# Performance work log

Measured on AMD Instinct MI355X. Metric: run time of the kernel, lower is better.

Reference implementation:

```python
import jax, jax.numpy as jnp
import numpy as np

# ---- config (matches init_kwargs) ----
NUM_HEADS = 8
HEAD_DIM = 48
IN_CH = 384
OUT_CH = 384
AGENTS_HW = (7, 7)
CLUSTERS_HW = (2, 2)
NUM_MODULES = 2          # ['PartitionalClustering', 'FuzzyClustering']
N_GROUPS = 1 + 2 * NUM_MODULES   # p + (k, v) per module
D = NUM_HEADS * HEAD_DIM          # 384
NUM_CLUSTERS = CLUSTERS_HW[0] * CLUSTERS_HW[1]   # 4 per module
NUM_ALL_CLUSTERS = NUM_MODULES * NUM_CLUSTERS    # 8
EPS = 1e-6


def adaptive_avg_pool(x, oh, ow):
    # x: [b, c, H, W], H % oh == 0, W % ow == 0 -> exact block mean
    b, c, H, W = x.shape
    return x.reshape(b, c, oh, H // oh, ow, W // ow).mean(axis=(3, 5))


def setup_inputs() -> dict:
    key = jax.random.key(0)
    ks = jax.random.split(key, 6)
    B, H, W = 16, 56, 56
    x = jax.random.normal(ks[0], (B, IN_CH, H, W), dtype=jnp.float32)
    # proj: 1x1 linear in_channels -> N_GROUPS * D
    proj_w = jax.random.normal(ks[1], (N_GROUPS * D, IN_CH), dtype=jnp.float32) * (IN_CH ** -0.5)
    proj_b = jnp.zeros((N_GROUPS * D,), dtype=jnp.float32)
    sim_alpha = jnp.ones((NUM_ALL_CLUSTERS,), dtype=jnp.float32)
    sim_beta = jnp.zeros((NUM_ALL_CLUSTERS,), dtype=jnp.float32)
    proj2_w = jax.random.normal(ks[2], (OUT_CH, D), dtype=jnp.float32) * (D ** -0.5)
    proj2_b = jnp.zeros((OUT_CH,), dtype=jnp.float32)
    return {"x": x, "proj_w": proj_w, "proj_b": proj_b,
            "sim_alpha": sim_alpha, "sim_beta": sim_beta,
            "proj2_w": proj2_w, "proj2_b": proj2_b}


def _cluster_attention(i, k, v, kc, vc):
    # k: [b, c, Na] agent keys; v: [b, Na, c] agent values
    # kc, vc: [b, M, c] cluster centroids (keys / values)
    c = k.shape[1]
    scores = jnp.einsum('bmc,bcn->bmn', kc, k) / jnp.sqrt(jnp.float32(c))  # [b, M, Na]
    if i == 0:  # PartitionalClustering: attend over tokens per centroid
        attn = jax.nn.softmax(scores, axis=-1)
        agg = jnp.einsum('bmn,bnc->bmc', attn, v)
    else:       # FuzzyClustering: soft membership over clusters, normalized average
        memb = jax.nn.softmax(scores, axis=1)                              # over clusters
        agg = jnp.einsum('bmn,bnc->bmc', memb, v) / (memb.sum(axis=-1, keepdims=True) + EPS)
    return agg + vc  # with_cluster_bias=True


def reference(x, proj_w, proj_b, sim_alpha, sim_beta, proj2_w, proj2_b):
    B, C, H, W = x.shape
    # proj (1x1 linear over channels)
    y = jnp.einsum('bchw,oc->bohw', x, proj_w) + proj_b[None, :, None, None]
    y = y.reshape(B, N_GROUPS, D, H, W).transpose(1, 0, 2, 3, 4)
    b = B * NUM_HEADS
    c = HEAD_DIM
    y = y.reshape(N_GROUPS, b, c, H, W)
    p, r = y[0], y[1:]
    r = r.reshape(NUM_MODULES, 2, b, c, H, W)

    ah, aw = AGENTS_HW
    na = ah * aw
    agg_list = []
    for i in range(NUM_MODULES):  # fixed small structural loop
        k_full, v_full = r[i, 0], r[i, 1]
        kc = adaptive_avg_pool(k_full, *CLUSTERS_HW).reshape(b, c, NUM_CLUSTERS).transpose(0, 2, 1)
        vc = adaptive_avg_pool(v_full, *CLUSTERS_HW).reshape(b, c, NUM_CLUSTERS).transpose(0, 2, 1)
        k = adaptive_avg_pool(k_full, ah, aw).reshape(b, c, na)             # [b, c, Na]
        v = adaptive_avg_pool(v_full, ah, aw).reshape(b, c, na).transpose(0, 2, 1)  # [b, Na, c]
        agg_list.append(_cluster_attention(i, k, v, kc, vc))
    agg = jnp.concatenate(agg_list, axis=1)  # [b, M_all, c]

    p_agents = adaptive_avg_pool(p, ah, aw).reshape(b, c, na)  # [b, c, Na]
    # cosine similarity between centroid aggregates and query tokens
    agg_n = agg / (jnp.linalg.norm(agg, axis=-1, keepdims=True) + EPS)
    p_n = p_agents / (jnp.linalg.norm(p_agents, axis=1, keepdims=True) + EPS)
    sim = jnp.einsum('bmc,bcn->bmn', agg_n, p_n)  # [b, M_all, Na]
    similarity = sim_alpha[None, :, None] * sim + sim_beta[None, :, None]
    assignment = jax.nn.softmax(similarity, axis=1)  # over clusters

    out = jnp.einsum('bmc,bmn->bcn', agg, assignment)  # [b, c, Na]
    out = out.reshape(b, c, ah, aw)
    # bilinear upsample (half-pixel centers == torch align_corners=False)
    out = jax.image.resize(out, (b, c, H, W), method='linear')
    out = out.reshape(B, D, H, W)
    out = jnp.einsum('bdhw,od->bohw', out, proj2_w) + proj2_b[None, :, None, None]
    return out
```

## Files before the change

kernel.cpp:

```cpp
#include <hip/hip_runtime.h>
#include <math.h>

#define CIN    384
#define NPIX   3136

typedef float vf4 __attribute__((ext_vector_type(4)));
typedef __attribute__((ext_vector_type(4))) float f32x4;
typedef __attribute__((ext_vector_type(8))) short bf16x8;
typedef __attribute__((ext_vector_type(8))) unsigned short u16x8;

__device__ __forceinline__ unsigned short f2bf(float f) {
    unsigned u = __float_as_uint(f);
    u = (u + 0x7FFF + ((u >> 16) & 1)) >> 16;
    return (unsigned short)u;
}
__device__ __forceinline__ float bf2f(unsigned short h) {
    return __uint_as_float(((unsigned)h) << 16);
}

__global__ __launch_bounds__(256) void k_front(const float* __restrict__ x,
                                               const float* __restrict__ W,
                                               unsigned short* __restrict__ Xhi,
                                               unsigned short* __restrict__ Xlo,
                                               unsigned short* __restrict__ Whi,
                                               unsigned short* __restrict__ Wlo) {
    int blk = blockIdx.x;
    int t = threadIdx.x;
    if (blk >= 6144) {
        int i = (blk - 6144) * 256 + t;
        float w = W[i];
        unsigned short hi = f2bf(w);
        Whi[i] = hi;
        Wlo[i] = f2bf(w - bf2f(hi));
        return;
    }
    int Bi = blk / CIN;
    int ch = blk - Bi * CIN;
    __shared__ float ps[56][14];
    __shared__ float s14[14][14];
    const float* xp = x + (size_t)(Bi * CIN + ch) * NPIX;
    for (int p = t; p < 784; p += 256) {
        int row = p / 14, cb = p % 14;
        const vf4 v = __builtin_nontemporal_load(
            reinterpret_cast<const vf4*>(xp + row * 56 + cb * 4));
        ps[row][cb] = v.x + v.y + v.z + v.w;
    }
    __syncthreads();
    if (t < 196) {
        int ri = t / 14, cb = t % 14;
        s14[ri][cb] = ps[4*ri][cb] + ps[4*ri+1][cb] + ps[4*ri+2][cb] + ps[4*ri+3][cb];
    }
    __syncthreads();
    if (t < 49) {
        int i = t / 7, j = t % 7;
        float s = (s14[2*i][2*j] + s14[2*i][2*j+1] + s14[2*i+1][2*j] + s14[2*i+1][2*j+1])
                  * (1.0f / 64.0f);
        int p = Bi * 49 + t;
        unsigned short hi = f2bf(s);
        Xhi[(size_t)p * 384 + ch] = hi;
        Xlo[(size_t)p * 384 + ch] = f2bf(s - bf2f(hi));
    } else if (t >= 64 && t < 68) {
        int m = t - 64;
        int mi = m / 2, mj = m % 2;
        float s = 0.f;
        for (int ri = 7*mi; ri < 7*mi + 7; ++ri)
            for (int cb = 7*mj; cb < 7*mj + 7; ++cb)
                s += s14[ri][cb];
        s *= (1.0f / 784.0f);
        int p = 784 + Bi * 4 + m;
        unsigned short hi = f2bf(s);
        Xhi[(size_t)p * 384 + ch] = hi;
        Xlo[(size_t)p * 384 + ch] = f2bf(s - bf2f(hi));
    }
}

__global__ __launch_bounds__(512) void k_fuse(
        const unsigned short* __restrict__ Whi, const unsigned short* __restrict__ Wlo,
        const unsigned short* __restrict__ Xhi, const unsigned short* __restrict__ Xlo,
        const float* __restrict__ proj_b,
        const float* __restrict__ alpha, const float* __restrict__ beta,
        float* __restrict__ osT) {
    int bb = blockIdx.x;
    int Bi = bb >> 3, head = bb & 7;
    __shared__ float yT[16560];
    __shared__ float e0[4][49], memb[4][49];
    __shared__ float rowmax0[4], esum0[4], msum[4];
    __shared__ float agg[8][48];
    __shared__ float anorm[8], pnorm[49];
    __shared__ float simL[8][49];
    __shared__ float assignW[8][49];
    unsigned short* sAh = (unsigned short*)yT;
    unsigned short* sAl = sAh + 9600;
    unsigned short* sBh = sAl + 9600;
    unsigned short* sBl = sBh + 2560;
    int t = threadIdx.x;
    int lane = t & 63, w = t >> 6;
    int fr = lane & 15, fq = lane >> 4;

    int row0 = t >> 2, ko0 = (t & 3) * 8;
    int g0 = row0 / 48, cc0 = row0 - g0 * 48;
    size_t aoff0 = (size_t)(g0 * 384 + head * 48 + cc0) * 384 + ko0;
    int c1 = t + 512;
    int row1 = c1 >> 2, ko1 = (c1 & 3) * 8;
    int g1 = row1 / 48, cc1 = row1 - g1 * 48;
    size_t aoff1 = (size_t)(g1 * 384 + head * 48 + cc1) * 384 + ko1;
    int bko = (t & 3) * 8;
    int brow = t >> 2;
    int bp = brow < 49 ? Bi * 49 + brow : 784 + Bi * 4 + (brow - 49);
    size_t boff = (size_t)bp * 384 + bko;

    u16x8 rAh0, rAl0, rAh1, rAl1, rBh, rBl;
    rAh0 = *(const u16x8*)(Whi + aoff0);
    rAl0 = *(const u16x8*)(Wlo + aoff0);
    if (t < 448) { rAh1 = *(const u16x8*)(Whi + aoff1); rAl1 = *(const u16x8*)(Wlo + aoff1); }
    if (t < 212) { rBh  = *(const u16x8*)(Xhi + boff);  rBl  = *(const u16x8*)(Xlo + boff); }

    f32x4 acc[2][4] = {};
    for (int step = 0; step < 12; ++step) {
        *(u16x8*)&sAh[row0 * 40 + ko0] = rAh0;
        *(u16x8*)&sAl[row0 * 40 + ko0] = rAl0;
        if (t < 448) {
            *(u16x8*)&sAh[row1 * 40 + ko1] = rAh1;
            *(u16x8*)&sAl[row1 * 40 + ko1] = rAl1;
        }
        if (t < 212) {
            *(u16x8*)&sBh[brow * 40 + bko] = rBh;
            *(u16x8*)&sBl[brow * 40 + bko] = rBl;
        }
        __syncthreads();
        if (step < 11) {
            int k0 = (step + 1) * 32;
            rAh0 = *(const u16x8*)(Whi + aoff0 + k0);
            rAl0 = *(const u16x8*)(Wlo + aoff0 + k0);
            if (t < 448) { rAh1 = *(const u16x8*)(Whi + aoff1 + k0); rAl1 = *(const u16x8*)(Wlo + aoff1 + k0); }
            if (t < 212) { rBh  = *(const u16x8*)(Xhi + boff + k0);  rBl  = *(const u16x8*)(Xlo + boff + k0); }
        }
        bf16x8 bh[4], bl[4];
#pragma unroll
        for (int nt = 0; nt < 4; ++nt) {
            int r = nt * 16 + fr;
            bh[nt] = *(const bf16x8*)&sBh[r * 40 + fq * 8];
            bl[nt] = *(const bf16x8*)&sBl[r * 40 + fq * 8];
        }
#pragma unroll
        for (int mi = 0; mi < 2; ++mi) {
            int mt = 2 * w + mi;
            if (mt < 15) {
                int r = mt * 16 + fr;
                bf16x8 ah = *(const bf16x8*)&sAh[r * 40 + fq * 8];
                bf16x8 al = *(const bf16x8*)&sAl[r * 40 + fq * 8];
#pragma unroll
                for (int nt = 0; nt < 4; ++nt) {
                    acc[mi][nt] = __builtin_amdgcn_mfma_f32_16x16x32_bf16(ah, bh[nt], acc[mi][nt], 0, 0, 0);
                    acc[mi][nt] = __builtin_amdgcn_mfma_f32_16x16x32_bf16(ah, bl[nt], acc[mi][nt], 0, 0, 0);
                    acc[mi][nt] = __builtin_amdgcn_mfma_f32_16x16x32_bf16(al, bh[nt], acc[mi][nt], 0, 0, 0);
                }
            }
        }
        __syncthreads();
    }
#pragma unroll
    for (int mi = 0; mi < 2; ++mi) {
        int mt = 2 * w + mi;
        if (mt < 15) {
#pragma unroll
            for (int j = 0; j < 4; ++j) {
                int m = mt * 16 + fq * 4 + j;
                int g = m / 48, cc = m - g * 48;
                float bb = proj_b[g * 384 + head * 48 + cc];
#pragma unroll
                for (int nt = 0; nt < 4; ++nt)
                    yT[m * 69 + nt * 16 + fr] = acc[mi][nt][j] + bb;
            }
        }
    }
    __syncthreads();

    const float scale = 0.14433756729740643f;
    if (t < 392) {
        int i = t / 196, r = t % 196;
        int m = r / 49, n = r % 49;
        int rbase = 48 + 96 * i;
        float s = 0.f;
        for (int cc = 0; cc < 48; ++cc)
            s += yT[(rbase + cc) * 69 + 49 + m] * yT[(rbase + cc) * 69 + n];
        s *= scale;
        if (i == 0) e0[m][n] = s; else memb[m][n] = s;
    }
    __syncthreads();
    if (t < 4) {
        float mx = -1e30f;
        for (int n = 0; n < 49; ++n) mx = fmaxf(mx, e0[t][n]);
        rowmax0[t] = mx;
    }
    __syncthreads();
    if (t < 196) { int m = t / 49, n = t % 49; e0[m][n] = expf(e0[m][n] - rowmax0[m]); }
    __syncthreads();
    if (t < 4) { float s = 0.f; for (int n = 0; n < 49; ++n) s += e0[t][n]; esum0[t] = s; }
    if (t >= 64 && t < 113) {
        int n = t - 64;
        float a0 = memb[0][n], a1 = memb[1][n], a2 = memb[2][n], a3 = memb[3][n];
        float mx = fmaxf(fmaxf(a0, a1), fmaxf(a2, a3));
        float x0 = expf(a0 - mx), x1 = expf(a1 - mx), x2 = expf(a2 - mx), x3 = expf(a3 - mx);
        float s = x0 + x1 + x2 + x3;
        memb[0][n] = x0 / s; memb[1][n] = x1 / s; memb[2][n] = x2 / s; memb[3][n] = x3 / s;
    }
    __syncthreads();
    if (t < 4) { float s = 0.f; for (int n = 0; n < 49; ++n) s += memb[t][n]; msum[t] = s; }
    __syncthreads();
    if (t < 384) {
        int row = t / 48, cc = t % 48;
        float a = 0.f;
        if (row < 4) {
            const float* vr = &yT[(96 + cc) * 69];
            for (int n = 0; n < 49; ++n) a += e0[row][n] * vr[n];
            agg[row][cc] = a / esum0[row] + vr[49 + row];
        } else {
            int m = row - 4;
            const float* vr = &yT[(192 + cc) * 69];
            for (int n = 0; n < 49; ++n) a += memb[m][n] * vr[n];
            agg[row][cc] = a / (msum[m] + 1e-6f) + vr[49 + m];
        }
    }
    __syncthreads();
    if (t < 8) {
        float s = 0.f;
        for (int cc = 0; cc < 48; ++cc) { float a = agg[t][cc]; s += a * a; }
        anorm[t] = sqrtf(s) + 1e-6f;
    }
    if (t >= 64 && t < 113) {
        int n = t - 64; float s = 0.f;
        for (int cc = 0; cc < 48; ++cc) { float a = yT[cc * 69 + n]; s += a * a; }
        pnorm[n] = sqrtf(s) + 1e-6f;
    }
    __syncthreads();
    if (t < 392) {
        int m = t / 49, n = t - m * 49;
        float dot = 0.f;
        for (int cc = 0; cc < 48; ++cc) dot += agg[m][cc] * yT[cc * 69 + n];
        simL[m][n] = alpha[m] * (dot / (anorm[m] * pnorm[n])) + beta[m];
    }
    __syncthreads();
    if (t < 49) {
        int n = t;
        float mx = -1e30f, e[8];
        for (int m = 0; m < 8; ++m) mx = fmaxf(mx, simL[m][n]);
        float ssum = 0.f;
        for (int m = 0; m < 8; ++m) { e[m] = expf(simL[m][n] - mx); ssum += e[m]; }
        float inv = 1.f / ssum;
        for (int m = 0; m < 8; ++m) assignW[m][n] = e[m] * inv;
    }
    __syncthreads();
    for (int idx = t; idx < 2352; idx += 512) {
        int n = idx / 48, cc = idx - n * 48;
        float s = 0.f;
        for (int m = 0; m < 8; ++m) s += agg[m][cc] * assignW[m][n];
        osT[((size_t)(Bi * 49 + n)) * 384 + head * 48 + cc] = s;
    }
}

__global__ __launch_bounds__(256) void k_upf(const float* __restrict__ osT,
                                             const float* __restrict__ W2,
                                             const float* __restrict__ b2,
                                             float* __restrict__ out) {
    int blk = blockIdx.x;
    int Bi = blk / 96, cg = blk - Bi * 96;
    int ch0 = cg * 4;
    __shared__ float W2L[4 * 388];
    __shared__ float OsL[49 * 100];
    __shared__ float zL[4][52];
    __shared__ float tmp[4][56][8];
    int t = threadIdx.x;
    for (int i = t; i < 1536; i += 256)
        W2L[(i / 384) * 388 + (i % 384)] = W2[(size_t)ch0 * 384 + i];
    int c = t & 3, n = t >> 2;
    float acc = 0.f;
    for (int kc = 0; kc < 4; ++kc) {
        __syncthreads();
        for (int i = t; i < 49 * 24; i += 256) {
            int nn = i / 24, j = i - nn * 24;
            float4 f = *reinterpret_cast<const float4*>(
                osT + ((size_t)(Bi * 49 + nn)) * 384 + kc * 96 + j * 4);
            *reinterpret_cast<float4*>(&OsL[nn * 100 + j * 4]) = f;
        }
        __syncthreads();
        if (t < 196) {
            const float* wrow = W2L + c * 388 + kc * 96;
            const float* orow = OsL + n * 100;
#pragma unroll
            for (int j = 0; j < 24; ++j) {
                float4 wv = *reinterpret_cast<const float4*>(wrow + j * 4);
                float4 ov = *reinterpret_cast<const float4*>(orow + j * 4);
                acc += wv.x * ov.x + wv.y * ov.y + wv.z * ov.z + wv.w * ov.w;
            }
        }
    }
    __syncthreads();
    if (t < 196) zL[c][n] = acc + b2[ch0 + c];
    __syncthreads();
    for (int idx = t; idx < 1568; idx += 256) {
        int cc = idx / 392, rem = idx - cc * 392;
        int h = rem / 7, iw = rem - h * 7;
        float sh = (h - 3.5f) * 0.125f;
        int ih0; float fh;
        if (sh <= 0.f)      { ih0 = 0; fh = 0.f; }
        else if (sh >= 6.f) { ih0 = 6; fh = 0.f; }
        else                { ih0 = (int)sh; fh = sh - (float)ih0; }
        int ih1 = min(ih0 + 1, 6);
        float z0 = zL[cc][ih0 * 7 + iw];
        tmp[cc][h][iw] = z0 + fh * (zL[cc][ih1 * 7 + iw] - z0);
    }
    __syncthreads();
    size_t obase = ((size_t)(Bi * 384 + ch0)) * (size_t)NPIX;
    for (int q = t; q < 3136; q += 256) {
        int cc = q / 784, rem = q - cc * 784;
        int h = rem / 14, qw = rem - h * 14;
        const float* tr = &tmp[cc][h][0];
        vf4 o4;
#pragma unroll
        for (int j = 0; j < 4; ++j) {
            int w = qw * 4 + j;
            float sw = (w - 3.5f) * 0.125f;
            int iw0; float fw;
            if (sw <= 0.f)      { iw0 = 0; fw = 0.f; }
            else if (sw >= 6.f) { iw0 = 6; fw = 0.f; }
            else                { iw0 = (int)sw; fw = sw - (float)iw0; }
            int iw1 = min(iw0 + 1, 6);
            float t0 = tr[iw0];
            o4[j] = t0 + fw * (tr[iw1] - t0);
        }
        __builtin_nontemporal_store(o4,
            reinterpret_cast<vf4*>(out + obase + (size_t)q * 4));
    }
}

extern "C" void kernel_launch(void* const* d_in, const int* in_sizes, int n_in,
                              void* d_out, int out_size, void* d_ws, size_t ws_size,
                              hipStream_t stream) {
    const float* x      = (const float*)d_in[0];
    const float* proj_w = (const float*)d_in[1];
    const float* proj_b = (const float*)d_in[2];
    const float* alpha  = (const float*)d_in[3];
    const float* beta   = (const float*)d_in[4];
    const float* w2     = (const float*)d_in[5];
    const float* b2     = (const float*)d_in[6];
    float* out = (float*)d_out;
    float* ws  = (float*)d_ws;

    float* osT = ws;
    unsigned short* Whi = (unsigned short*)(ws + (size_t)301056);
    unsigned short* Wlo = (unsigned short*)(ws + (size_t)669696);
    unsigned short* Xhi = (unsigned short*)(ws + (size_t)1038336);
    unsigned short* Xlo = (unsigned short*)(ws + (size_t)1210368);

    k_front<<<dim3(9024), 256, 0, stream>>>(x, proj_w, Xhi, Xlo, Whi, Wlo);
    k_fuse <<<dim3(128),  512, 0, stream>>>(Whi, Wlo, Xhi, Xlo, proj_b, alpha, beta, osT);
    k_upf  <<<dim3(1536), 256, 0, stream>>>(osT, w2, b2, out);
}
```

Before: 81.17 us.

## Move proj2 GEMM onto split-bf16 MFMA kernel ahead of upsample

After: 74.36 us. 8.4% less time.

```diff
diff --git a/kernel.cpp b/kernel.cpp
--- a/kernel.cpp
+++ b/kernel.cpp
@@ -19,19 +19,30 @@
 }
 
 __global__ __launch_bounds__(256) void k_front(const float* __restrict__ x,
-                                               const float* __restrict__ W,
+                                               const float* __restrict__ W1,
+                                               const float* __restrict__ W2,
                                                unsigned short* __restrict__ Xhi,
                                                unsigned short* __restrict__ Xlo,
-                                               unsigned short* __restrict__ Whi,
-                                               unsigned short* __restrict__ Wlo) {
+                                               unsigned short* __restrict__ Whi1,
+                                               unsigned short* __restrict__ Wlo1,
+                                               unsigned short* __restrict__ Whi2,
+                                               unsigned short* __restrict__ Wlo2) {
     int blk = blockIdx.x;
     int t = threadIdx.x;
+    if (blk >= 9024) {
+        int i = (blk - 9024) * 256 + t;
+        float w = W2[i];
+        unsigned short hi = f2bf(w);
+        Whi2[i] = hi;
+        Wlo2[i] = f2bf(w - bf2f(hi));
+        return;
+    }
     if (blk >= 6144) {
         int i = (blk - 6144) * 256 + t;
-        float w = W[i];
+        float w = W1[i];
         unsigned short hi = f2bf(w);
-        Whi[i] = hi;
-        Wlo[i] = f2bf(w - bf2f(hi));
+        Whi1[i] = hi;
+        Wlo1[i] = f2bf(w - bf2f(hi));
         return;
     }
     int Bi = blk / CIN;
@@ -79,7 +90,7 @@
         const unsigned short* __restrict__ Xhi, const unsigned short* __restrict__ Xlo,
         const float* __restrict__ proj_b,
         const float* __restrict__ alpha, const float* __restrict__ beta,
-        float* __restrict__ osT) {
+        unsigned short* __restrict__ osThi, unsigned short* __restrict__ osTlo) {
     int bb = blockIdx.x;
     int Bi = bb >> 3, head = bb & 7;
     __shared__ float yT[16560];
@@ -251,55 +262,84 @@
         for (int m = 0; m < 8; ++m) assignW[m][n] = e[m] * inv;
     }
     __syncthreads();
-    for (int idx = t; idx < 2352; idx += 512) {
+    for (int idx = t; idx < 3072; idx += 512) {
         int n = idx / 48, cc = idx - n * 48;
         float s = 0.f;
-        for (int m = 0; m < 8; ++m) s += agg[m][cc] * assignW[m][n];
-        osT[((size_t)(Bi * 49 + n)) * 384 + head * 48 + cc] = s;
-    }
-}
-
-__global__ __launch_bounds__(256) void k_upf(const float* __restrict__ osT,
-                                             const float* __restrict__ W2,
+        if (n < 49)
+            for (int m = 0; m < 8; ++m) s += agg[m][cc] * assignW[m][n];
+        size_t o = ((size_t)(Bi * 64 + n)) * 384 + head * 48 + cc;
+        unsigned short hi = f2bf(s);
+        osThi[o] = hi;
+        osTlo[o] = f2bf(s - bf2f(hi));
+    }
+}
+
+__global__ __launch_bounds__(512) void k_gemm2m(
+        const unsigned short* __restrict__ Whi2, const unsigned short* __restrict__ Wlo2,
+        const unsigned short* __restrict__ osThi, const unsigned short* __restrict__ osTlo,
+        float* __restrict__ z) {
+    int blk = blockIdx.x;
+    int Bi = blk / 3, rg = blk - Bi * 3;
+    __shared__ unsigned short sAh[128 * 40], sAl[128 * 40];
+    __shared__ unsigned short sBh[64 * 40],  sBl[64 * 40];
+    int t = threadIdx.x;
+    int lane = t & 63, w = t >> 6;
+    int fr = lane & 15, fq = lane >> 4;
+    int arow = t >> 2, ako = (t & 3) * 8;
+    size_t aoff = (size_t)(rg * 128 + arow) * 384 + ako;
+    int brow = (t & 255) >> 2, bko = (t & 3) * 8;
+    size_t boff = ((size_t)(Bi * 64 + brow)) * 384 + bko;
+    f32x4 acc[4] = {};
+    for (int k0 = 0; k0 < 384; k0 += 32) {
+        *(u16x8*)&sAh[arow * 40 + ako] = *(const u16x8*)(Whi2 + aoff + k0);
+        *(u16x8*)&sAl[arow * 40 + ako] = *(const u16x8*)(Wlo2 + aoff + k0);
+        if (t < 256) {
+            *(u16x8*)&sBh[brow * 40 + bko] = *(const u16x8*)(osThi + boff + k0);
+            *(u16x8*)&sBl[brow * 40 + bko] = *(const u16x8*)(osTlo + boff + k0);
+        }
+        __syncthreads();
+        int r = w * 16 + fr;
+        bf16x8 ah = *(const bf16x8*)&sAh[r * 40 + fq * 8];
+        bf16x8 al = *(const bf16x8*)&sAl[r * 40 + fq * 8];
+#pragma unroll
+        for (int nt = 0; nt < 4; ++nt) {
+            int rb = nt * 16 + fr;
+            bf16x8 bh = *(const bf16x8*)&sBh[rb * 40 + fq * 8];
+            bf16x8 bl = *(const bf16x8*)&sBl[rb * 40 + fq * 8];
+            acc[nt] = __builtin_amdgcn_mfma_f32_16x16x32_bf16(ah, bh, acc[nt], 0, 0, 0);
+            acc[nt] = __builtin_amdgcn_mfma_f32_16x16x32_bf16(ah, bl, acc[nt], 0, 0, 0);
+            acc[nt] = __builtin_amdgcn_mfma_f32_16x16x32_bf16(al, bh, acc[nt], 0, 0, 0);
+        }
+        __syncthreads();
+    }
+#pragma unroll
+    for (int j = 0; j < 4; ++j) {
+        int ch = rg * 128 + w * 16 + fq * 4 + j;
+#pragma unroll
+        for (int nt = 0; nt < 4; ++nt) {
+            int col = nt * 16 + fr;
+            if (col < 49)
+                z[((size_t)(Bi * 384 + ch)) * 52 + col] = acc[nt][j];
+        }
+    }
+}
+
+__global__ __launch_bounds__(256) void k_up4(const float* __restrict__ z,
                                              const float* __restrict__ b2,
                                              float* __restrict__ out) {
     int blk = blockIdx.x;
     int Bi = blk / 96, cg = blk - Bi * 96;
     int ch0 = cg * 4;
-    __shared__ float W2L[4 * 388];
-    __shared__ float OsL[49 * 100];
     __shared__ float zL[4][52];
     __shared__ float tmp[4][56][8];
     int t = threadIdx.x;
-    for (int i = t; i < 1536; i += 256)
-        W2L[(i / 384) * 388 + (i % 384)] = W2[(size_t)ch0 * 384 + i];
-    int c = t & 3, n = t >> 2;
-    float acc = 0.f;
-    for (int kc = 0; kc < 4; ++kc) {
-        __syncthreads();
-        for (int i = t; i < 49 * 24; i += 256) {
-            int nn = i / 24, j = i - nn * 24;
-            float4 f = *reinterpret_cast<const float4*>(
-                osT + ((size_t)(Bi * 49 + nn)) * 384 + kc * 96 + j * 4);
-            *reinterpret_cast<float4*>(&OsL[nn * 100 + j * 4]) = f;
-        }
-        __syncthreads();
-        if (t < 196) {
-            const float* wrow = W2L + c * 388 + kc * 96;
-            const float* orow = OsL + n * 100;
-#pragma unroll
-            for (int j = 0; j < 24; ++j) {
-                float4 wv = *reinterpret_cast<const float4*>(wrow + j * 4);
-                float4 ov = *reinterpret_cast<const float4*>(orow + j * 4);
-                acc += wv.x * ov.x + wv.y * ov.y + wv.z * ov.z + wv.w * ov.w;
-            }
-        }
-    }
-    __syncthreads();
-    if (t < 196) zL[c][n] = acc + b2[ch0 + c];
+    if (t < 196) {
+        int c = t / 49, n = t - c * 49;
+        zL[c][n] = z[((size_t)(Bi * 384 + ch0 + c)) * 52 + n] + b2[ch0 + c];
+    }
     __syncthreads();
     for (int idx = t; idx < 1568; idx += 256) {
-        int cc = idx / 392, rem = idx - cc * 392;
+        int c = idx / 392, rem = idx - c * 392;
         int h = rem / 7, iw = rem - h * 7;
         float sh = (h - 3.5f) * 0.125f;
         int ih0; float fh;
@@ -307,15 +347,15 @@
         else if (sh >= 6.f) { ih0 = 6; fh = 0.f; }
         else                { ih0 = (int)sh; fh = sh - (float)ih0; }
         int ih1 = min(ih0 + 1, 6);
-        float z0 = zL[cc][ih0 * 7 + iw];
-        tmp[cc][h][iw] = z0 + fh * (zL[cc][ih1 * 7 + iw] - z0);
+        float z0 = zL[c][ih0 * 7 + iw];
+        tmp[c][h][iw] = z0 + fh * (zL[c][ih1 * 7 + iw] - z0);
     }
     __syncthreads();
     size_t obase = ((size_t)(Bi * 384 + ch0)) * (size_t)NPIX;
     for (int q = t; q < 3136; q += 256) {
-        int cc = q / 784, rem = q - cc * 784;
+        int c = q / 784, rem = q - c * 784;
         int h = rem / 14, qw = rem - h * 14;
-        const float* tr = &tmp[cc][h][0];
+        const float* tr = &tmp[c][h][0];
         vf4 o4;
 #pragma unroll
         for (int j = 0; j < 4; ++j) {
@@ -347,13 +387,18 @@
     float* out = (float*)d_out;
     float* ws  = (float*)d_ws;
 
-    float* osT = ws;
-    unsigned short* Whi = (unsigned short*)(ws + (size_t)301056);
-    unsigned short* Wlo = (unsigned short*)(ws + (size_t)669696);
-    unsigned short* Xhi = (unsigned short*)(ws + (size_t)1038336);
-    unsigned short* Xlo = (unsigned short*)(ws + (size_t)1210368);
-
-    k_front<<<dim3(9024), 256, 0, stream>>>(x, proj_w, Xhi, Xlo, Whi, Wlo);
-    k_fuse <<<dim3(128),  512, 0, stream>>>(Whi, Wlo, Xhi, Xlo, proj_b, alpha, beta, osT);
-    k_upf  <<<dim3(1536), 256, 0, stream>>>(osT, w2, b2, out);
-}
+    float* z = ws;
+    unsigned short* Whi1  = (unsigned short*)(ws + (size_t)319488);
+    unsigned short* Wlo1  = (unsigned short*)(ws + (size_t)688128);
+    unsigned short* Xhi   = (unsigned short*)(ws + (size_t)1056768);
+    unsigned short* Xlo   = (unsigned short*)(ws + (size_t)1228800);
+    unsigned short* Whi2  = (unsigned short*)(ws + (size_t)1400832);
+    unsigned short* Wlo2  = (unsigned short*)(ws + (size_t)1474560);
+    unsigned short* osThi = (unsigned short*)(ws + (size_t)1548288);
+    unsigned short* osTlo = (unsigned short*)(ws + (size_t)1744896);
+
+    k_front <<<dim3(9600), 256, 0, stream>>>(x, proj_w, w2, Xhi, Xlo, Whi1, Wlo1, Whi2, Wlo2);
+    k_fuse  <<<dim3(128),  512, 0, stream>>>(Whi1, Wlo1, Xhi, Xlo, proj_b, alpha, beta, osThi, osTlo);
+    k_gemm2m<<<dim3(48),   512, 0, stream>>>(Whi2, Wlo2, osThi, osTlo, z);
+    k_up4   <<<dim3(1536), 256, 0, stream>>>(z, b2, out);
+}
```
